# Optimization experiments

Measured on AMD Instinct MI355X. Metric: run time of the kernel, lower is better.

Reference implementation:

```python
import jax, jax.numpy as jnp
import numpy as np

ITER_ROUTING = 3
FINAL_LAMBDA = 0.01
EPS = 1e-9

N = 4
CHILD_SPACE = 12
KERNEL = 3
STRIDE = 1
CHILD_CAPS = 16
PARENT_CAPS = 32
POSE = 16


def _routing_map(child_space, k, s):
    # (child_space^2, parent_space^2) binary map: child c feeds parent p.
    parent_space = (child_space - k) // s + 1
    m = np.zeros((child_space * child_space, parent_space * parent_space), np.float32)
    for pr in range(parent_space):
        for pc in range(parent_space):
            p = pr * parent_space + pc
            for r in range(k):
                for c in range(k):
                    m[(pr * s + r) * child_space + (pc * s + c), p] = 1.0
    return m


def setup_inputs() -> dict:
    key = jax.random.key(0)
    k1, k2, k3, k4 = jax.random.split(key, 4)
    parent_space = (CHILD_SPACE - KERNEL) // STRIDE + 1
    kk = KERNEL * KERNEL
    votes = jax.random.normal(k1, (N * parent_space * parent_space, kk * CHILD_CAPS, PARENT_CAPS, POSE), jnp.float32)
    acts = jax.random.uniform(k2, (N * parent_space * parent_space, kk * CHILD_CAPS, 1), dtype=jnp.float32)
    beta_v = jax.random.normal(k3, (1, 1, 1, 1, PARENT_CAPS, 1), jnp.float32)
    beta_a = jax.random.normal(k4, (1, 1, 1, 1, PARENT_CAPS, 1), jnp.float32)
    srm = jnp.asarray(_routing_map(CHILD_SPACE, KERNEL, STRIDE))
    return {"votes_ij": votes, "activations_i": acts, "beta_v": beta_v, "beta_a": beta_a,
            "spatial_routing_matrix": srm, "batch_size": N, "kk": kk}


def _em_routing(votes_ij, activations_i, beta_v, beta_a, srm, batch_size, kk):
    Nb = batch_size
    C2, P2 = srm.shape  # child_space^2, parent_space^2
    P = int(round(P2 ** 0.5))
    K_total, O, ch = votes_ij.shape[1], votes_ij.shape[2], votes_ij.shape[3]
    child_caps = K_total // kk

    votes = votes_ij.reshape(Nb, P, P, K_total, O, ch)
    act_i = activations_i.reshape(Nb, P, P, K_total, 1, 1)

    # children per parent, ascending child index (stable argsort on -1/0 values)
    cidx = jnp.argsort(-srm, axis=0)[:kk].T           # (P2, kk)
    seg = cidx.reshape(-1)                            # (P2*kk,) child id per (parent, slot)
    ppc = jnp.sum(srm, axis=1)                        # parents-per-child, (C2,)
    # init_rr: 1 / (parents_per_child * parent_caps + 1e-9), gathered per parent slot
    rr0 = (1.0 / (ppc[cidx] * O + 1e-9)).reshape(1, P, P, kk, 1, 1)
    rr = jnp.broadcast_to(rr0, (1, P, P, kk, child_caps, O)).reshape(1, P, P, K_total, O, 1)

    layer_norm_factor = 100.0 / (float(K_total) / float(O))

    def m_step(rr, it):
        lam = FINAL_LAMBDA * (1.0 - 0.95 ** (it + 1))
        rr_prime = rr * act_i                                            # (N,P,P,K,O,1)
        rr_prime_sum = jnp.sum(rr_prime, axis=-3, keepdims=True)         # (N,P,P,1,O,1)
        mean_j = jnp.sum(rr_prime * votes, axis=-3, keepdims=True) / (rr_prime_sum + EPS)
        var_j = jnp.sum(rr_prime * jnp.square(votes - mean_j), axis=-3, keepdims=True) / (rr_prime_sum + EPS)
        cost_j_h = (beta_v + 0.5 * jnp.log(var_j + EPS)) * rr_prime_sum * layer_norm_factor
        cost_j = jnp.sum(cost_j_h, axis=-1, keepdims=True)               # (N,P,P,1,O,1)
        cost_mean = jnp.mean(cost_j, axis=-2, keepdims=True)
        cost_stdv = jnp.sqrt(jnp.sum(jnp.square(cost_j - cost_mean), axis=-2, keepdims=True) / O)
        act_j = jax.nn.sigmoid(lam * (beta_a + (cost_mean - cost_j) / (cost_stdv + EPS)))
        return act_j, mean_j, var_j

    def e_step(act_j, mean_j, var_j):
        # log N(vote; mean_j, var_j) per parent + log activation
        o_p0 = -jnp.sum(jnp.square(votes - mean_j) / (2.0 * var_j), axis=-1, keepdims=True)
        o_p2 = -0.5 * jnp.sum(jnp.log(2.0 * np.pi * var_j), axis=-1, keepdims=True)
        zz = jnp.log(act_j + EPS) + o_p0 + o_p2                          # (N,P,P,K,O,1)
        # softmax over ALL parents of each child (spatial kk slots x parent_caps),
        # done via segment reductions keyed by child id (== sparse/softmax/dense of original)
        z = jnp.moveaxis(zz.reshape(Nb, P2 * kk, child_caps, O), 1, 0)   # (P2*kk, N, cc, O)
        m = jax.ops.segment_max(jnp.max(z, axis=-1), seg, num_segments=C2)  # (C2, N, cc)
        m = jnp.where(jnp.isinf(m), 0.0, m)
        e = jnp.exp(z - m[seg][..., None])
        denom = jax.ops.segment_sum(jnp.sum(e, axis=-1), seg, num_segments=C2)
        rr_new = e / denom[seg][..., None]
        return jnp.moveaxis(rr_new, 0, 1).reshape(Nb, P, P, K_total, O, 1)

    for it in range(ITER_ROUTING):
        act_j, mean_j, var_j = m_step(rr, it)
        if it < ITER_ROUTING - 1:
            rr = e_step(act_j, mean_j, var_j)

    poses_j = mean_j[:, :, :, 0]        # (N,P,P,O,16)
    activations_j = act_j[:, :, :, 0]   # (N,P,P,O,1)
    return poses_j, activations_j


def reference(votes_ij, activations_i, beta_v, beta_a, spatial_routing_matrix, batch_size, kk):
    return _em_routing(votes_ij, activations_i, beta_v, beta_a, spatial_routing_matrix, batch_size, kk)
```

## Files before the change

kernel.cpp:

```cpp
#include <hip/hip_runtime.h>
#include <math.h>

#define NB     4
#define P      10
#define P2     100
#define CS     12
#define CCAPS  16
#define KTOT   144
#define O      32
#define POSE   16
#define VSZ    73728
#define EPSF   1e-9f
#define LNF    22.2222222222222222f
#define TWO_PI 6.28318530717958647f
#define NBP    400
#define NKQ    3
#define KPU    48
#define SUNITS (NBP*NKQ)
#define EUNITS (NB*CS*CS*2)

#define LAM0 0.0005f
#define LAM1 0.000975f
#define LAM2 0.00142625f

__device__ float g_rr [NBP*KTOT*O];
__device__ float g_zz [NBP*KTOT*O];
__device__ float g_m1 [SUNITS*512];
__device__ float g_m2 [SUNITS*512];
__device__ float g_sv [SUNITS*O];

__device__ __forceinline__ int npar(int x) {
    int a = x + 1, b = CS - x;
    int m = a < 3 ? a : 3;
    return m < b ? m : b;
}

template<bool FIRST>
__global__ __launch_bounds__(256)
void s_kernel(const float* __restrict__ votes, const float* __restrict__ acts)
{
    __shared__ float actl[KPU];
    __shared__ __align__(16) float rrp[KPU*O];
    __shared__ float4 lm1[256];
    __shared__ float4 lm2[256];
    __shared__ float  lss[256];

    const int tid = threadIdx.x;
    const int u   = blockIdx.x;
    const int bp  = u / NKQ;
    const int kq  = u - bp * NKQ;
    const int k0  = kq * KPU;
    const int ks  = tid >> 7;
    const int q   = tid & 127;
    const int o   = q >> 2;

    if (tid < KPU) actl[tid] = acts[bp * KTOT + k0 + tid];
    __syncthreads();

    for (int f = tid; f < KPU * O / 4; f += 256) {
        int kl = f >> 3;
        float4 r4;
        if (FIRST) {
            int kg = k0 + kl, kslot = kg >> 4;
            int kr = kslot / 3, kc = kslot - kr * 3;
            int p = bp % P2, pr = p / P, pc = p - pr * P;
            float ppc = (float)(npar(pr + kr) * npar(pc + kc));
            float r = actl[kl] / (ppc * 32.0f + EPSF);
            r4 = make_float4(r, r, r, r);
        } else {
            r4 = ((const float4*)(g_rr + (size_t)bp * (KTOT * O) + k0 * O))[f];
            float a = actl[kl];
            r4.x *= a; r4.y *= a; r4.z *= a; r4.w *= a;
        }
        ((float4*)rrp)[f] = r4;
    }
    __syncthreads();

    const float* vb  = votes + (size_t)bp * VSZ + (size_t)(k0 + ks * 24) * 512 + q * 4;
    const float* rr0 = rrp + (ks * 24) * O + o;
    float  s  = 0.f;
    float4 m1 = make_float4(0.f, 0.f, 0.f, 0.f);
    float4 m2 = make_float4(0.f, 0.f, 0.f, 0.f);
    #pragma unroll 8
    for (int i = 0; i < 24; ++i) {
        float  rp = rr0[i * O];
        float4 v  = *(const float4*)(vb + i * 512);
        s += rp;
        m1.x += rp * v.x;       m1.y += rp * v.y;
        m1.z += rp * v.z;       m1.w += rp * v.w;
        m2.x += rp * v.x * v.x; m2.y += rp * v.y * v.y;
        m2.z += rp * v.z * v.z; m2.w += rp * v.w * v.w;
    }
    lm1[tid] = m1; lm2[tid] = m2; lss[tid] = s;
    __syncthreads();

    if (tid < 128) {
        float4 a = lm1[tid], b = lm1[tid + 128];
        m1 = make_float4(a.x + b.x, a.y + b.y, a.z + b.z, a.w + b.w);
        a = lm2[tid]; b = lm2[tid + 128];
        m2 = make_float4(a.x + b.x, a.y + b.y, a.z + b.z, a.w + b.w);
        s = lss[tid] + lss[tid + 128];
        ((float4*)g_m1)[u * 128 + tid] = m1;
        ((float4*)g_m2)[u * 128 + tid] = m2;
        if ((tid & 3) == 0) g_sv[u * O + (tid >> 2)] = s;
    }
}

__device__ __forceinline__ void finish_bp(int bp, int tid, float lam,
                                          const float* __restrict__ beta_v,
                                          const float* __restrict__ beta_a,
                                          float4& mean, float4& i2,
                                          float& aj, float& lv2out,
                                          float* costl )
{
    const int o = tid >> 2, c4 = tid & 3;
    float4 m1 = make_float4(0.f, 0.f, 0.f, 0.f);
    float4 m2 = make_float4(0.f, 0.f, 0.f, 0.f);
    float  s  = 0.f;
    #pragma unroll
    for (int j = 0; j < NKQ; ++j) {
        float4 a = ((const float4*)g_m1)[(bp * NKQ + j) * 128 + tid];
        float4 b = ((const float4*)g_m2)[(bp * NKQ + j) * 128 + tid];
        m1.x += a.x; m1.y += a.y; m1.z += a.z; m1.w += a.w;
        m2.x += b.x; m2.y += b.y; m2.z += b.z; m2.w += b.w;
        s += g_sv[(bp * NKQ + j) * O + o];
    }
    float denom = s + EPSF;
    mean = make_float4(m1.x / denom, m1.y / denom, m1.z / denom, m1.w / denom);
    float4 var;
    var.x = fmaxf(m2.x / denom - mean.x * mean.x, 1e-30f);
    var.y = fmaxf(m2.y / denom - mean.y * mean.y, 1e-30f);
    var.z = fmaxf(m2.z / denom - mean.z * mean.z, 1e-30f);
    var.w = fmaxf(m2.w / denom - mean.w * mean.w, 1e-30f);
    i2 = make_float4(0.5f / var.x, 0.5f / var.y, 0.5f / var.z, 0.5f / var.w);
    float lve = logf(var.x + EPSF) + logf(var.y + EPSF)
              + logf(var.z + EPSF) + logf(var.w + EPSF);
    float lv2 = logf(TWO_PI * var.x) + logf(TWO_PI * var.y)
              + logf(TWO_PI * var.z) + logf(TWO_PI * var.w);
    lve += __shfl_xor(lve, 1); lve += __shfl_xor(lve, 2);
    lv2 += __shfl_xor(lv2, 1); lv2 += __shfl_xor(lv2, 2);
    lv2out = lv2;
    if (c4 == 0) costl[o] = (16.f * beta_v[o] + 0.5f * lve) * s * LNF;
    __syncthreads();
    float cm = 0.f;
    #pragma unroll
    for (int i = 0; i < O; ++i) cm += costl[i];
    cm *= (1.f / 32.f);
    float sq = 0.f;
    #pragma unroll
    for (int i = 0; i < O; ++i) { float d = costl[i] - cm; sq += d * d; }
    float cstd = sqrtf(sq * (1.f / 32.f));
    aj = 1.f / (1.f + expf(-lam * (beta_a[o] + (cm - costl[o]) / (cstd + EPSF))));
}

__global__ __launch_bounds__(256)
void zf_kernel(const float* __restrict__ votes,
               const float* __restrict__ beta_v,
               const float* __restrict__ beta_a, float lam)
{
    __shared__ float4 ml[128];
    __shared__ float4 il[128];
    __shared__ float  zl[O];
    __shared__ float  costl[O];
    __shared__ __align__(16) float zzl[KPU*O];

    const int tid = threadIdx.x;
    const int u   = blockIdx.x;
    const int bp  = u / NKQ;
    const int kq  = u - bp * NKQ;
    const int k0  = kq * KPU;
    const int ks  = tid >> 7;
    const int q   = tid & 127;
    const int o   = q >> 2;
    const int c4  = q & 3;

    {
        float4 mean, i2; float aj, lv2;
        if (tid < 128) {
            finish_bp(bp, tid, lam, beta_v, beta_a, mean, i2, aj, lv2, costl);
            ml[tid] = mean; il[tid] = i2;
            if ((tid & 3) == 0)
                zl[tid >> 2] = logf(aj + EPSF) - 0.5f * lv2;
        } else {
            __syncthreads();
        }
    }
    __syncthreads();

    const float* vb = votes + (size_t)bp * VSZ + (size_t)(k0 + ks * 24) * 512 + q * 4;
    float4 m  = ml[q];
    float4 iv = il[q];
    float  zp = zl[o];
    #pragma unroll 8
    for (int i = 0; i < 24; ++i) {
        float4 v = *(const float4*)(vb + i * 512);
        float dx = v.x - m.x, dy = v.y - m.y, dz = v.z - m.z, dw = v.w - m.w;
        float t = dx * dx * iv.x + dy * dy * iv.y + dz * dz * iv.z + dw * dw * iv.w;
        t += __shfl_xor(t, 1); t += __shfl_xor(t, 2);
        if (c4 == 0) zzl[(ks * 24 + i) * O + o] = zp - t;
    }
    __syncthreads();
    float4* dst = (float4*)(g_zz + (size_t)bp * (KTOT * O) + k0 * O);
    for (int f = tid; f < KPU * O / 4; f += 256)
        dst[f] = ((float4*)zzl)[f];
}

__global__ __launch_bounds__(256)
void f_last_kernel(const float* __restrict__ beta_v,
                   const float* __restrict__ beta_a,
                   float* __restrict__ out, float lam)
{
    __shared__ float costl[O];
    const int tid = threadIdx.x;
    const int bp  = blockIdx.x;
    float4 mean, i2; float aj, lv2;
    if (tid < 128) {
        finish_bp(bp, tid, lam, beta_v, beta_a, mean, i2, aj, lv2, costl);
        ((float4*)out)[bp * 128 + tid] = mean;
        if ((tid & 3) == 0)
            out[(size_t)NBP * 512 + bp * O + (tid >> 2)] = aj;
    } else {
        __syncthreads();
    }
}

__global__ __launch_bounds__(256)
void e_kernel()
{
    const int tid = threadIdx.x;
    const int u   = blockIdx.x;
    const int b   = u / (CS * CS * 2);
    int r = u - b * (CS * CS * 2);
    const int child = r >> 1, half = r & 1;
    const int cr = child / CS, cl = child - cr * CS;
    const int cc = half * 8 + (tid >> 5), o = tid & 31;

    float zz[9];
    float vmax = -1e30f;
    #pragma unroll
    for (int kr = 0; kr < 3; ++kr) {
        int pr_ = cr - kr;
        #pragma unroll
        for (int kc = 0; kc < 3; ++kc) {
            int pc_ = cl - kc, si = kr * 3 + kc;
            float z = -1e30f;
            if (pr_ >= 0 && pr_ < P && pc_ >= 0 && pc_ < P) {
                int bpp = b * P2 + pr_ * P + pc_;
                z = g_zz[(size_t)bpp * (KTOT * O) + (si * CCAPS + cc) * O + o];
            }
            zz[si] = z;
            vmax = fmaxf(vmax, z);
        }
    }
    vmax = fmaxf(vmax, __shfl_xor(vmax, 1));
    vmax = fmaxf(vmax, __shfl_xor(vmax, 2));
    vmax = fmaxf(vmax, __shfl_xor(vmax, 4));
    vmax = fmaxf(vmax, __shfl_xor(vmax, 8));
    vmax = fmaxf(vmax, __shfl_xor(vmax, 16));

    float ps = 0.f;
    #pragma unroll
    for (int si = 0; si < 9; ++si) {
        float e = (zz[si] > -1e29f) ? expf(zz[si] - vmax) : 0.f;
        zz[si] = e;
        ps += e;
    }
    ps += __shfl_xor(ps, 1);
    ps += __shfl_xor(ps, 2);
    ps += __shfl_xor(ps, 4);
    ps += __shfl_xor(ps, 8);
    ps += __shfl_xor(ps, 16);
    float inv = 1.f / ps;

    #pragma unroll
    for (int kr = 0; kr < 3; ++kr) {
        int pr_ = cr - kr;
        #pragma unroll
        for (int kc = 0; kc < 3; ++kc) {
            int pc_ = cl - kc, si = kr * 3 + kc;
            if (pr_ >= 0 && pr_ < P && pc_ >= 0 && pc_ < P) {
                int bpp = b * P2 + pr_ * P + pc_;
                g_rr[(size_t)bpp * (KTOT * O) + (si * CCAPS + cc) * O + o] = zz[si] * inv;
            }
        }
    }
}

extern "C" void kernel_launch(void* const* d_in, const int* in_sizes, int n_in,
                              void* d_out, int out_size, void* d_ws, size_t ws_size,
                              hipStream_t stream)
{
    (void)in_sizes; (void)n_in; (void)out_size; (void)d_ws; (void)ws_size;

    const float* votes = (const float*)d_in[0];
    const float* acts  = (const float*)d_in[1];
    const float* bv    = (const float*)d_in[2];
    const float* ba    = (const float*)d_in[3];
    float* out = (float*)d_out;

    dim3 t(256);
    s_kernel<true ><<<dim3(SUNITS), t, 0, stream>>>(votes, acts);
    zf_kernel<<<dim3(SUNITS), t, 0, stream>>>(votes, bv, ba, LAM0);
    e_kernel<<<dim3(EUNITS), t, 0, stream>>>();

    s_kernel<false><<<dim3(SUNITS), t, 0, stream>>>(votes, acts);
    zf_kernel<<<dim3(SUNITS), t, 0, stream>>>(votes, bv, ba, LAM1);
    e_kernel<<<dim3(EUNITS), t, 0, stream>>>();

    s_kernel<false><<<dim3(SUNITS), t, 0, stream>>>(votes, acts);
    f_last_kernel<<<dim3(NBP), t, 0, stream>>>(bv, ba, out, LAM2);
}
```

Before: 276.8 us.

## Cache votes as fp16 in workspace and read half-precision copy in later passes

The first M-step pass now also writes an fp16 copy of the votes tensor into the workspace. Every later pass (the z computations and the second and third M-steps) reads 8 halves per thread instead of 4 floats, so those passes move half as many bytes. Thread mapping and the reductions are reworked to fit the new 8-element vectors. The cost is lower precision in the means, variances and log-likelihoods, plus an extra fp16 write during the first pass.

Result: faster. 257.5 us (-7.0%).

```diff
diff --git a/kernel.cpp b/kernel.cpp
--- a/kernel.cpp
+++ b/kernel.cpp
@@ -1,4 +1,5 @@
 #include <hip/hip_runtime.h>
+#include <hip/hip_fp16.h>
 #include <math.h>
 
 #define NB     4
@@ -35,9 +36,18 @@
     return m < b ? m : b;
 }
 
-template<bool FIRST>
-__global__ __launch_bounds__(256)
-void s_kernel(const float* __restrict__ votes, const float* __restrict__ acts)
+__device__ __forceinline__ void up8(uint4 u, float* f) {
+    float2 a = __half22float2(*(__half2*)&u.x);
+    float2 b = __half22float2(*(__half2*)&u.y);
+    float2 c = __half22float2(*(__half2*)&u.z);
+    float2 d = __half22float2(*(__half2*)&u.w);
+    f[0] = a.x; f[1] = a.y; f[2] = b.x; f[3] = b.y;
+    f[4] = c.x; f[5] = c.y; f[6] = d.x; f[7] = d.y;
+}
+
+__global__ __launch_bounds__(256)
+void v_kernel(const float* __restrict__ votes, const float* __restrict__ acts,
+              __half* __restrict__ hv)
 {
     __shared__ float actl[KPU];
     __shared__ __align__(16) float rrp[KPU*O];
@@ -59,24 +69,17 @@
 
     for (int f = tid; f < KPU * O / 4; f += 256) {
         int kl = f >> 3;
-        float4 r4;
-        if (FIRST) {
-            int kg = k0 + kl, kslot = kg >> 4;
-            int kr = kslot / 3, kc = kslot - kr * 3;
-            int p = bp % P2, pr = p / P, pc = p - pr * P;
-            float ppc = (float)(npar(pr + kr) * npar(pc + kc));
-            float r = actl[kl] / (ppc * 32.0f + EPSF);
-            r4 = make_float4(r, r, r, r);
-        } else {
-            r4 = ((const float4*)(g_rr + (size_t)bp * (KTOT * O) + k0 * O))[f];
-            float a = actl[kl];
-            r4.x *= a; r4.y *= a; r4.z *= a; r4.w *= a;
-        }
-        ((float4*)rrp)[f] = r4;
+        int kg = k0 + kl, kslot = kg >> 4;
+        int kr = kslot / 3, kc = kslot - kr * 3;
+        int p = bp % P2, pr = p / P, pc = p - pr * P;
+        float ppc = (float)(npar(pr + kr) * npar(pc + kc));
+        float r = actl[kl] / (ppc * 32.0f + EPSF);
+        ((float4*)rrp)[f] = make_float4(r, r, r, r);
     }
     __syncthreads();
 
     const float* vb  = votes + (size_t)bp * VSZ + (size_t)(k0 + ks * 24) * 512 + q * 4;
+    __half*      hb  = hv    + (size_t)bp * VSZ + (size_t)(k0 + ks * 24) * 512 + q * 4;
     const float* rr0 = rrp + (ks * 24) * O + o;
     float  s  = 0.f;
     float4 m1 = make_float4(0.f, 0.f, 0.f, 0.f);
@@ -90,6 +93,12 @@
         m1.z += rp * v.z;       m1.w += rp * v.w;
         m2.x += rp * v.x * v.x; m2.y += rp * v.y * v.y;
         m2.z += rp * v.z * v.z; m2.w += rp * v.w * v.w;
+        __half2 ha = __floats2half2_rn(v.x, v.y);
+        __half2 hbv = __floats2half2_rn(v.z, v.w);
+        uint2 st;
+        st.x = *(unsigned int*)&ha;
+        st.y = *(unsigned int*)&hbv;
+        *(uint2*)(hb + i * 512) = st;
     }
     lm1[tid] = m1; lm2[tid] = m2; lss[tid] = s;
     __syncthreads();
@@ -103,6 +112,80 @@
         ((float4*)g_m1)[u * 128 + tid] = m1;
         ((float4*)g_m2)[u * 128 + tid] = m2;
         if ((tid & 3) == 0) g_sv[u * O + (tid >> 2)] = s;
+    }
+}
+
+__global__ __launch_bounds__(256)
+void s16_kernel(const __half* __restrict__ hv, const float* __restrict__ acts)
+{
+    __shared__ float actl[KPU];
+    __shared__ __align__(16) float rrp[KPU*O];
+    __shared__ float4 lm1[512];
+    __shared__ float4 lm2[512];
+    __shared__ float  lss[256];
+
+    const int tid = threadIdx.x;
+    const int u   = blockIdx.x;
+    const int bp  = u / NKQ;
+    const int kq  = u - bp * NKQ;
+    const int k0  = kq * KPU;
+    const int ks  = tid >> 6;
+    const int qp  = tid & 63;
+    const int o   = qp >> 1;
+
+    if (tid < KPU) actl[tid] = acts[bp * KTOT + k0 + tid];
+    __syncthreads();
+
+    for (int f = tid; f < KPU * O / 4; f += 256) {
+        int kl = f >> 3;
+        float4 r4 = ((const float4*)(g_rr + (size_t)bp * (KTOT * O) + k0 * O))[f];
+        float a = actl[kl];
+        r4.x *= a; r4.y *= a; r4.z *= a; r4.w *= a;
+        ((float4*)rrp)[f] = r4;
+    }
+    __syncthreads();
+
+    const __half* vb = hv + (size_t)bp * VSZ + (size_t)(k0 + ks * 12) * 512 + qp * 8;
+    const float* rr0 = rrp + (ks * 12) * O + o;
+    float s = 0.f;
+    float m1[8], m2[8];
+    #pragma unroll
+    for (int j = 0; j < 8; ++j) { m1[j] = 0.f; m2[j] = 0.f; }
+    #pragma unroll 4
+    for (int i = 0; i < 12; ++i) {
+        float rp = rr0[i * O];
+        uint4 u4 = *(const uint4*)(vb + i * 512);
+        float f[8]; up8(u4, f);
+        s += rp;
+        #pragma unroll
+        for (int j = 0; j < 8; ++j) {
+            m1[j] += rp * f[j];
+            m2[j] += rp * f[j] * f[j];
+        }
+    }
+    lm1[tid*2]   = make_float4(m1[0], m1[1], m1[2], m1[3]);
+    lm1[tid*2+1] = make_float4(m1[4], m1[5], m1[6], m1[7]);
+    lm2[tid*2]   = make_float4(m2[0], m2[1], m2[2], m2[3]);
+    lm2[tid*2+1] = make_float4(m2[4], m2[5], m2[6], m2[7]);
+    lss[tid] = s;
+    __syncthreads();
+
+    if (tid < 64) {
+        #pragma unroll
+        for (int j = 0; j < 2; ++j) {
+            float4 a0 = lm1[(tid)*2+j],       a1 = lm1[(64+tid)*2+j];
+            float4 a2 = lm1[(128+tid)*2+j],   a3 = lm1[(192+tid)*2+j];
+            float4 r = make_float4(a0.x+a1.x+a2.x+a3.x, a0.y+a1.y+a2.y+a3.y,
+                                   a0.z+a1.z+a2.z+a3.z, a0.w+a1.w+a2.w+a3.w);
+            ((float4*)g_m1)[u * 128 + tid*2 + j] = r;
+            float4 b0 = lm2[(tid)*2+j],       b1 = lm2[(64+tid)*2+j];
+            float4 b2 = lm2[(128+tid)*2+j],   b3 = lm2[(192+tid)*2+j];
+            float4 r2 = make_float4(b0.x+b1.x+b2.x+b3.x, b0.y+b1.y+b2.y+b3.y,
+                                    b0.z+b1.z+b2.z+b3.z, b0.w+b1.w+b2.w+b3.w);
+            ((float4*)g_m2)[u * 128 + tid*2 + j] = r2;
+        }
+        float sr = lss[tid] + lss[64+tid] + lss[128+tid] + lss[192+tid];
+        if ((tid & 1) == 0) g_sv[u * O + (tid >> 1)] = sr;
     }
 }
 
@@ -154,9 +237,9 @@
 }
 
 __global__ __launch_bounds__(256)
-void zf_kernel(const float* __restrict__ votes,
-               const float* __restrict__ beta_v,
-               const float* __restrict__ beta_a, float lam)
+void zf16_kernel(const __half* __restrict__ hv,
+                 const float* __restrict__ beta_v,
+                 const float* __restrict__ beta_a, float lam)
 {
     __shared__ float4 ml[128];
     __shared__ float4 il[128];
@@ -169,10 +252,10 @@
     const int bp  = u / NKQ;
     const int kq  = u - bp * NKQ;
     const int k0  = kq * KPU;
-    const int ks  = tid >> 7;
-    const int q   = tid & 127;
-    const int o   = q >> 2;
-    const int c4  = q & 3;
+    const int ks  = tid >> 6;
+    const int qp  = tid & 63;
+    const int o   = qp >> 1;
+    const int h   = qp & 1;
 
     {
         float4 mean, i2; float aj, lv2;
@@ -187,17 +270,20 @@
     }
     __syncthreads();
 
-    const float* vb = votes + (size_t)bp * VSZ + (size_t)(k0 + ks * 24) * 512 + q * 4;
-    float4 m  = ml[q];
-    float4 iv = il[q];
+    const __half* vb = hv + (size_t)bp * VSZ + (size_t)(k0 + ks * 12) * 512 + qp * 8;
+    float4 mA = ml[o*4 + h*2], mB = ml[o*4 + h*2 + 1];
+    float4 iA = il[o*4 + h*2], iB = il[o*4 + h*2 + 1];
     float  zp = zl[o];
-    #pragma unroll 8
-    for (int i = 0; i < 24; ++i) {
-        float4 v = *(const float4*)(vb + i * 512);
-        float dx = v.x - m.x, dy = v.y - m.y, dz = v.z - m.z, dw = v.w - m.w;
-        float t = dx * dx * iv.x + dy * dy * iv.y + dz * dz * iv.z + dw * dw * iv.w;
-        t += __shfl_xor(t, 1); t += __shfl_xor(t, 2);
-        if (c4 == 0) zzl[(ks * 24 + i) * O + o] = zp - t;
+    #pragma unroll 4
+    for (int i = 0; i < 12; ++i) {
+        uint4 u4 = *(const uint4*)(vb + i * 512);
+        float f[8]; up8(u4, f);
+        float d0 = f[0]-mA.x, d1 = f[1]-mA.y, d2 = f[2]-mA.z, d3 = f[3]-mA.w;
+        float d4 = f[4]-mB.x, d5 = f[5]-mB.y, d6 = f[6]-mB.z, d7 = f[7]-mB.w;
+        float t = d0*d0*iA.x + d1*d1*iA.y + d2*d2*iA.z + d3*d3*iA.w
+                + d4*d4*iB.x + d5*d5*iB.y + d6*d6*iB.z + d7*d7*iB.w;
+        t += __shfl_xor(t, 1);
+        if (h == 0) zzl[(ks * 12 + i) * O + o] = zp - t;
     }
     __syncthreads();
     float4* dst = (float4*)(g_zz + (size_t)bp * (KTOT * O) + k0 * O);
@@ -290,23 +376,24 @@
                               void* d_out, int out_size, void* d_ws, size_t ws_size,
                               hipStream_t stream)
 {
-    (void)in_sizes; (void)n_in; (void)out_size; (void)d_ws; (void)ws_size;
+    (void)in_sizes; (void)n_in; (void)out_size; (void)ws_size;
 
     const float* votes = (const float*)d_in[0];
     const float* acts  = (const float*)d_in[1];
     const float* bv    = (const float*)d_in[2];
     const float* ba    = (const float*)d_in[3];
     float* out = (float*)d_out;
+    __half* hv = (__half*)d_ws;
 
     dim3 t(256);
-    s_kernel<true ><<<dim3(SUNITS), t, 0, stream>>>(votes, acts);
-    zf_kernel<<<dim3(SUNITS), t, 0, stream>>>(votes, bv, ba, LAM0);
+    v_kernel<<<dim3(SUNITS), t, 0, stream>>>(votes, acts, hv);
+    zf16_kernel<<<dim3(SUNITS), t, 0, stream>>>(hv, bv, ba, LAM0);
     e_kernel<<<dim3(EUNITS), t, 0, stream>>>();
 
-    s_kernel<false><<<dim3(SUNITS), t, 0, stream>>>(votes, acts);
-    zf_kernel<<<dim3(SUNITS), t, 0, stream>>>(votes, bv, ba, LAM1);
+    s16_kernel<<<dim3(SUNITS), t, 0, stream>>>(hv, acts);
+    zf16_kernel<<<dim3(SUNITS), t, 0, stream>>>(hv, bv, ba, LAM1);
     e_kernel<<<dim3(EUNITS), t, 0, stream>>>();
 
-    s_kernel<false><<<dim3(SUNITS), t, 0, stream>>>(votes, acts);
+    s16_kernel<<<dim3(SUNITS), t, 0, stream>>>(hv, acts);
     f_last_kernel<<<dim3(NBP), t, 0, stream>>>(bv, ba, out, LAM2);
 }
```

## Fuse E-step with next M-step stats per child and cache votes as fp16

Applied to the files above, without the earlier changes.

The routing pipeline is restructured. The first pass writes an fp16 copy of votes into the workspace. A per-child kernel then computes the log-likelihood, the softmax over all parents and the weighted partial moments in one pass, so the zz and rr round trips and the separate full-precision vote re-reads go away. Small per-parent finish kernels reduce the partials. Votes are read at half the bytes in later iterations, at the cost of fp16 precision loss in mean and variance, plus extra block-wide syncs inside a loop with possibly divergent bounds.

Measured after the change: 304.7 us. 10.1% more time.

```diff
diff --git a/kernel.cpp b/kernel.cpp
--- a/kernel.cpp
+++ b/kernel.cpp
@@ -1,4 +1,5 @@
 #include <hip/hip_runtime.h>
+#include <hip/hip_fp16.h>
 #include <math.h>
 
 #define NB     4
@@ -17,17 +18,21 @@
 #define NKQ    3
 #define KPU    48
 #define SUNITS (NBP*NKQ)
-#define EUNITS (NB*CS*CS*2)
+#define NCQ    2
+#define CZG    (NB*CS*CS*NCQ)
 
 #define LAM0 0.0005f
 #define LAM1 0.000975f
 #define LAM2 0.00142625f
 
-__device__ float g_rr [NBP*KTOT*O];
-__device__ float g_zz [NBP*KTOT*O];
 __device__ float g_m1 [SUNITS*512];
 __device__ float g_m2 [SUNITS*512];
 __device__ float g_sv [SUNITS*O];
+__device__ float g_pm [NBP*9*NCQ*1024];
+__device__ float g_ps [NBP*9*NCQ*32];
+__device__ float g_mean[NBP*512];
+__device__ float g_i2v [NBP*512];
+__device__ float g_zpre[NBP*O];
 
 __device__ __forceinline__ int npar(int x) {
     int a = x + 1, b = CS - x;
@@ -35,9 +40,18 @@
     return m < b ? m : b;
 }
 
-template<bool FIRST>
+__device__ __forceinline__ void up8(uint4 u, float* f) {
+    float2 a = __half22float2(*(__half2*)&u.x);
+    float2 b = __half22float2(*(__half2*)&u.y);
+    float2 c = __half22float2(*(__half2*)&u.z);
+    float2 d = __half22float2(*(__half2*)&u.w);
+    f[0] = a.x; f[1] = a.y; f[2] = b.x; f[3] = b.y;
+    f[4] = c.x; f[5] = c.y; f[6] = d.x; f[7] = d.y;
+}
+
 __global__ __launch_bounds__(256)
-void s_kernel(const float* __restrict__ votes, const float* __restrict__ acts)
+void v_kernel(const float* __restrict__ votes, const float* __restrict__ acts,
+              __half* __restrict__ hv)
 {
     __shared__ float actl[KPU];
     __shared__ __align__(16) float rrp[KPU*O];
@@ -59,24 +73,17 @@
 
     for (int f = tid; f < KPU * O / 4; f += 256) {
         int kl = f >> 3;
-        float4 r4;
-        if (FIRST) {
-            int kg = k0 + kl, kslot = kg >> 4;
-            int kr = kslot / 3, kc = kslot - kr * 3;
-            int p = bp % P2, pr = p / P, pc = p - pr * P;
-            float ppc = (float)(npar(pr + kr) * npar(pc + kc));
-            float r = actl[kl] / (ppc * 32.0f + EPSF);
-            r4 = make_float4(r, r, r, r);
-        } else {
-            r4 = ((const float4*)(g_rr + (size_t)bp * (KTOT * O) + k0 * O))[f];
-            float a = actl[kl];
-            r4.x *= a; r4.y *= a; r4.z *= a; r4.w *= a;
-        }
-        ((float4*)rrp)[f] = r4;
+        int kg = k0 + kl, kslot = kg >> 4;
+        int kr = kslot / 3, kc = kslot - kr * 3;
+        int p = bp % P2, pr = p / P, pc = p - pr * P;
+        float ppc = (float)(npar(pr + kr) * npar(pc + kc));
+        float r = actl[kl] / (ppc * 32.0f + EPSF);
+        ((float4*)rrp)[f] = make_float4(r, r, r, r);
     }
     __syncthreads();
 
     const float* vb  = votes + (size_t)bp * VSZ + (size_t)(k0 + ks * 24) * 512 + q * 4;
+    __half*      hb  = hv    + (size_t)bp * VSZ + (size_t)(k0 + ks * 24) * 512 + q * 4;
     const float* rr0 = rrp + (ks * 24) * O + o;
     float  s  = 0.f;
     float4 m1 = make_float4(0.f, 0.f, 0.f, 0.f);
@@ -90,6 +97,12 @@
         m1.z += rp * v.z;       m1.w += rp * v.w;
         m2.x += rp * v.x * v.x; m2.y += rp * v.y * v.y;
         m2.z += rp * v.z * v.z; m2.w += rp * v.w * v.w;
+        __half2 ha  = __floats2half2_rn(v.x, v.y);
+        __half2 hbv = __floats2half2_rn(v.z, v.w);
+        uint2 st;
+        st.x = *(unsigned int*)&ha;
+        st.y = *(unsigned int*)&hbv;
+        *(uint2*)(hb + i * 512) = st;
     }
     lm1[tid] = m1; lm2[tid] = m2; lss[tid] = s;
     __syncthreads();
@@ -106,14 +119,15 @@
     }
 }
 
-__device__ __forceinline__ void finish_bp(int bp, int tid, float lam,
-                                          const float* __restrict__ beta_v,
-                                          const float* __restrict__ beta_a,
-                                          float4& mean, float4& i2,
-                                          float& aj, float& lv2out,
-                                          float* costl )
-{
+__global__ __launch_bounds__(128)
+void f0_kernel(const float* __restrict__ beta_v,
+               const float* __restrict__ beta_a, float lam)
+{
+    __shared__ float costl[O];
+    const int tid = threadIdx.x;
     const int o = tid >> 2, c4 = tid & 3;
+    const int bp = blockIdx.x;
+
     float4 m1 = make_float4(0.f, 0.f, 0.f, 0.f);
     float4 m2 = make_float4(0.f, 0.f, 0.f, 0.f);
     float  s  = 0.f;
@@ -126,129 +140,83 @@
         s += g_sv[(bp * NKQ + j) * O + o];
     }
     float denom = s + EPSF;
-    mean = make_float4(m1.x / denom, m1.y / denom, m1.z / denom, m1.w / denom);
+    float4 mean = make_float4(m1.x/denom, m1.y/denom, m1.z/denom, m1.w/denom);
     float4 var;
-    var.x = fmaxf(m2.x / denom - mean.x * mean.x, 1e-30f);
-    var.y = fmaxf(m2.y / denom - mean.y * mean.y, 1e-30f);
-    var.z = fmaxf(m2.z / denom - mean.z * mean.z, 1e-30f);
-    var.w = fmaxf(m2.w / denom - mean.w * mean.w, 1e-30f);
-    i2 = make_float4(0.5f / var.x, 0.5f / var.y, 0.5f / var.z, 0.5f / var.w);
-    float lve = logf(var.x + EPSF) + logf(var.y + EPSF)
-              + logf(var.z + EPSF) + logf(var.w + EPSF);
-    float lv2 = logf(TWO_PI * var.x) + logf(TWO_PI * var.y)
-              + logf(TWO_PI * var.z) + logf(TWO_PI * var.w);
-    lve += __shfl_xor(lve, 1); lve += __shfl_xor(lve, 2);
-    lv2 += __shfl_xor(lv2, 1); lv2 += __shfl_xor(lv2, 2);
-    lv2out = lv2;
-    if (c4 == 0) costl[o] = (16.f * beta_v[o] + 0.5f * lve) * s * LNF;
+    var.x = fmaxf(m2.x/denom - mean.x*mean.x, 1e-30f);
+    var.y = fmaxf(m2.y/denom - mean.y*mean.y, 1e-30f);
+    var.z = fmaxf(m2.z/denom - mean.z*mean.z, 1e-30f);
+    var.w = fmaxf(m2.w/denom - mean.w*mean.w, 1e-30f);
+    float4 i2 = make_float4(0.5f/var.x, 0.5f/var.y, 0.5f/var.z, 0.5f/var.w);
+    float lve = logf(var.x+EPSF)+logf(var.y+EPSF)+logf(var.z+EPSF)+logf(var.w+EPSF);
+    float lv2 = logf(TWO_PI*var.x)+logf(TWO_PI*var.y)+logf(TWO_PI*var.z)+logf(TWO_PI*var.w);
+    lve += __shfl_xor(lve,1); lve += __shfl_xor(lve,2);
+    lv2 += __shfl_xor(lv2,1); lv2 += __shfl_xor(lv2,2);
+    if (c4 == 0) costl[o] = (16.f*beta_v[o] + 0.5f*lve) * s * LNF;
     __syncthreads();
     float cm = 0.f;
     #pragma unroll
     for (int i = 0; i < O; ++i) cm += costl[i];
-    cm *= (1.f / 32.f);
+    cm *= (1.f/32.f);
     float sq = 0.f;
     #pragma unroll
-    for (int i = 0; i < O; ++i) { float d = costl[i] - cm; sq += d * d; }
-    float cstd = sqrtf(sq * (1.f / 32.f));
-    aj = 1.f / (1.f + expf(-lam * (beta_a[o] + (cm - costl[o]) / (cstd + EPSF))));
+    for (int i = 0; i < O; ++i) { float d = costl[i]-cm; sq += d*d; }
+    float cstd = sqrtf(sq * (1.f/32.f));
+    float aj = 1.f/(1.f+expf(-lam*(beta_a[o] + (cm-costl[o])/(cstd+EPSF))));
+    ((float4*)g_mean)[bp*128+tid] = mean;
+    ((float4*)g_i2v)[bp*128+tid]  = i2;
+    if (c4 == 0) g_zpre[bp*O+o] = logf(aj+EPSF) - 0.5f*lv2;
 }
 
 __global__ __launch_bounds__(256)
-void zf_kernel(const float* __restrict__ votes,
-               const float* __restrict__ beta_v,
-               const float* __restrict__ beta_a, float lam)
-{
-    __shared__ float4 ml[128];
-    __shared__ float4 il[128];
-    __shared__ float  zl[O];
-    __shared__ float  costl[O];
-    __shared__ __align__(16) float zzl[KPU*O];
+void cz_kernel(const __half* __restrict__ hv, const float* __restrict__ acts)
+{
+    __shared__ float red[4*32*33];
 
     const int tid = threadIdx.x;
-    const int u   = blockIdx.x;
-    const int bp  = u / NKQ;
-    const int kq  = u - bp * NKQ;
-    const int k0  = kq * KPU;
-    const int ks  = tid >> 7;
-    const int q   = tid & 127;
-    const int o   = q >> 2;
-    const int c4  = q & 3;
-
-    {
-        float4 mean, i2; float aj, lv2;
-        if (tid < 128) {
-            finish_bp(bp, tid, lam, beta_v, beta_a, mean, i2, aj, lv2, costl);
-            ml[tid] = mean; il[tid] = i2;
-            if ((tid & 3) == 0)
-                zl[tid >> 2] = logf(aj + EPSF) - 0.5f * lv2;
-        } else {
-            __syncthreads();
-        }
-    }
-    __syncthreads();
-
-    const float* vb = votes + (size_t)bp * VSZ + (size_t)(k0 + ks * 24) * 512 + q * 4;
-    float4 m  = ml[q];
-    float4 iv = il[q];
-    float  zp = zl[o];
-    #pragma unroll 8
-    for (int i = 0; i < 24; ++i) {
-        float4 v = *(const float4*)(vb + i * 512);
-        float dx = v.x - m.x, dy = v.y - m.y, dz = v.z - m.z, dw = v.w - m.w;
-        float t = dx * dx * iv.x + dy * dy * iv.y + dz * dz * iv.z + dw * dw * iv.w;
-        t += __shfl_xor(t, 1); t += __shfl_xor(t, 2);
-        if (c4 == 0) zzl[(ks * 24 + i) * O + o] = zp - t;
-    }
-    __syncthreads();
-    float4* dst = (float4*)(g_zz + (size_t)bp * (KTOT * O) + k0 * O);
-    for (int f = tid; f < KPU * O / 4; f += 256)
-        dst[f] = ((float4*)zzl)[f];
-}
-
-__global__ __launch_bounds__(256)
-void f_last_kernel(const float* __restrict__ beta_v,
-                   const float* __restrict__ beta_a,
-                   float* __restrict__ out, float lam)
-{
-    __shared__ float costl[O];
-    const int tid = threadIdx.x;
-    const int bp  = blockIdx.x;
-    float4 mean, i2; float aj, lv2;
-    if (tid < 128) {
-        finish_bp(bp, tid, lam, beta_v, beta_a, mean, i2, aj, lv2, costl);
-        ((float4*)out)[bp * 128 + tid] = mean;
-        if ((tid & 3) == 0)
-            out[(size_t)NBP * 512 + bp * O + (tid >> 2)] = aj;
-    } else {
-        __syncthreads();
-    }
-}
-
-__global__ __launch_bounds__(256)
-void e_kernel()
-{
-    const int tid = threadIdx.x;
-    const int u   = blockIdx.x;
-    const int b   = u / (CS * CS * 2);
-    int r = u - b * (CS * CS * 2);
-    const int child = r >> 1, half = r & 1;
-    const int cr = child / CS, cl = child - cr * CS;
-    const int cc = half * 8 + (tid >> 5), o = tid & 31;
-
-    float zz[9];
+    const int ccl = tid >> 5;
+    const int o   = tid & 31;
+    const int blk = blockIdx.x;
+    const int ccq = blk & (NCQ-1);
+    const int bc  = blk / NCQ;
+    const int b   = bc / (CS*CS);
+    const int c   = bc - b*(CS*CS);
+    const int cr  = c / CS, cl = c - cr*CS;
+    const int cc  = ccq*8 + ccl;
+
+    int   bpps[9];
+    float ez[9];
+    float av[9];
     float vmax = -1e30f;
+
     #pragma unroll
     for (int kr = 0; kr < 3; ++kr) {
-        int pr_ = cr - kr;
         #pragma unroll
         for (int kc = 0; kc < 3; ++kc) {
-            int pc_ = cl - kc, si = kr * 3 + kc;
+            const int si  = kr*3 + kc;
+            const int pr_ = cr - kr, pc_ = cl - kc;
+            const bool ok = (pr_ >= 0 && pr_ < P && pc_ >= 0 && pc_ < P);
+            int bpp = ok ? (b*P2 + pr_*P + pc_) : -1;
+            bpps[si] = bpp;
             float z = -1e30f;
-            if (pr_ >= 0 && pr_ < P && pc_ >= 0 && pc_ < P) {
-                int bpp = b * P2 + pr_ * P + pc_;
-                z = g_zz[(size_t)bpp * (KTOT * O) + (si * CCAPS + cc) * O + o];
+            if (ok) {
+                const __half* vb = hv + (size_t)bpp*VSZ + (size_t)(si*16+cc)*512 + o*16;
+                uint4 u0 = *(const uint4*)(vb);
+                uint4 u1 = *(const uint4*)(vb + 8);
+                float f[16]; up8(u0, f); up8(u1, f + 8);
+                const float4* mm = (const float4*)(g_mean + (size_t)bpp*512 + o*16);
+                const float4* iv = (const float4*)(g_i2v  + (size_t)bpp*512 + o*16);
+                float t = 0.f;
+                #pragma unroll
+                for (int j4 = 0; j4 < 4; ++j4) {
+                    float4 m = mm[j4], w = iv[j4];
+                    float d0 = f[j4*4  ]-m.x, d1 = f[j4*4+1]-m.y;
+                    float d2 = f[j4*4+2]-m.z, d3 = f[j4*4+3]-m.w;
+                    t += d0*d0*w.x + d1*d1*w.y + d2*d2*w.z + d3*d3*w.w;
+                }
+                z = g_zpre[bpp*O + o] - t;
+                av[si] = acts[bpp*KTOT + si*16 + cc];
             }
-            zz[si] = z;
+            ez[si] = z;
             vmax = fmaxf(vmax, z);
         }
     }
@@ -257,12 +225,11 @@
     vmax = fmaxf(vmax, __shfl_xor(vmax, 4));
     vmax = fmaxf(vmax, __shfl_xor(vmax, 8));
     vmax = fmaxf(vmax, __shfl_xor(vmax, 16));
-
     float ps = 0.f;
     #pragma unroll
     for (int si = 0; si < 9; ++si) {
-        float e = (zz[si] > -1e29f) ? expf(zz[si] - vmax) : 0.f;
-        zz[si] = e;
+        float e = (ez[si] > -1e29f) ? expf(ez[si] - vmax) : 0.f;
+        ez[si] = e;
         ps += e;
     }
     ps += __shfl_xor(ps, 1);
@@ -270,19 +237,114 @@
     ps += __shfl_xor(ps, 4);
     ps += __shfl_xor(ps, 8);
     ps += __shfl_xor(ps, 16);
-    float inv = 1.f / ps;
-
-    #pragma unroll
-    for (int kr = 0; kr < 3; ++kr) {
-        int pr_ = cr - kr;
+    const float inv = 1.f / ps;
+
+    #pragma unroll
+    for (int si = 0; si < 9; ++si) {
+        const int bpp = bpps[si];
+        if (bpp >= 0) {
+            float rp = ez[si] * inv * av[si];
+            const __half* vb = hv + (size_t)bpp*VSZ + (size_t)(si*16+cc)*512 + o*16;
+            uint4 u0 = *(const uint4*)(vb);
+            uint4 u1 = *(const uint4*)(vb + 8);
+            float f[16]; up8(u0, f); up8(u1, f + 8);
+            float m1[16], m2[16];
+            #pragma unroll
+            for (int j = 0; j < 16; ++j) { m1[j] = rp*f[j]; m2[j] = rp*f[j]*f[j]; }
+            float s = rp;
+            #pragma unroll
+            for (int j = 0; j < 16; ++j) {
+                m1[j] += __shfl_xor(m1[j], 32);
+                m2[j] += __shfl_xor(m2[j], 32);
+            }
+            s += __shfl_xor(s, 32);
+            if ((ccl & 1) == 0) {
+                float* r = red + ((ccl >> 1)*32 + o)*33;
+                #pragma unroll
+                for (int j = 0; j < 16; ++j) { r[j] = m1[j]; r[16+j] = m2[j]; }
+                r[32] = s;
+            }
+            __syncthreads();
+            if (tid < 32) {
+                float* dst = g_pm + ((size_t)(bpp*9 + si)*NCQ + ccq)*1024;
+                float sa = 0.f;
+                #pragma unroll
+                for (int j4 = 0; j4 < 8; ++j4) {
+                    float4 acc = make_float4(0.f, 0.f, 0.f, 0.f);
+                    #pragma unroll
+                    for (int w = 0; w < 4; ++w) {
+                        const float* r = red + (w*32 + tid)*33 + j4*4;
+                        acc.x += r[0]; acc.y += r[1]; acc.z += r[2]; acc.w += r[3];
+                    }
+                    int half = j4 >> 2, j4l = j4 & 3;
+                    ((float4*)(dst + half*512))[tid*4 + j4l] = acc;
+                }
+                #pragma unroll
+                for (int w = 0; w < 4; ++w) sa += red[(w*32 + tid)*33 + 32];
+                g_ps[((bpp*9 + si)*NCQ + ccq)*32 + tid] = sa;
+            }
+            __syncthreads();
+        }
+    }
+}
+
+template<bool LAST>
+__global__ __launch_bounds__(128)
+void f12_kernel(const float* __restrict__ beta_v,
+                const float* __restrict__ beta_a,
+                float* __restrict__ out, float lam)
+{
+    __shared__ float costl[O];
+    const int tid = threadIdx.x;
+    const int o = tid >> 2, c4 = tid & 3;
+    const int bp = blockIdx.x;
+
+    float4 m1 = make_float4(0.f, 0.f, 0.f, 0.f);
+    float4 m2 = make_float4(0.f, 0.f, 0.f, 0.f);
+    float  s  = 0.f;
+    #pragma unroll
+    for (int si = 0; si < 9; ++si) {
         #pragma unroll
-        for (int kc = 0; kc < 3; ++kc) {
-            int pc_ = cl - kc, si = kr * 3 + kc;
-            if (pr_ >= 0 && pr_ < P && pc_ >= 0 && pc_ < P) {
-                int bpp = b * P2 + pr_ * P + pc_;
-                g_rr[(size_t)bpp * (KTOT * O) + (si * CCAPS + cc) * O + o] = zz[si] * inv;
-            }
+        for (int qq = 0; qq < NCQ; ++qq) {
+            const float* base = g_pm + ((size_t)(bp*9 + si)*NCQ + qq)*1024;
+            float4 a = ((const float4*)base)[tid];
+            float4 b = ((const float4*)(base + 512))[tid];
+            m1.x += a.x; m1.y += a.y; m1.z += a.z; m1.w += a.w;
+            m2.x += b.x; m2.y += b.y; m2.z += b.z; m2.w += b.w;
+            s += g_ps[((bp*9 + si)*NCQ + qq)*32 + o];
         }
+    }
+    float denom = s + EPSF;
+    float4 mean = make_float4(m1.x/denom, m1.y/denom, m1.z/denom, m1.w/denom);
+    float4 var;
+    var.x = fmaxf(m2.x/denom - mean.x*mean.x, 1e-30f);
+    var.y = fmaxf(m2.y/denom - mean.y*mean.y, 1e-30f);
+    var.z = fmaxf(m2.z/denom - mean.z*mean.z, 1e-30f);
+    var.w = fmaxf(m2.w/denom - mean.w*mean.w, 1e-30f);
+    float4 i2 = make_float4(0.5f/var.x, 0.5f/var.y, 0.5f/var.z, 0.5f/var.w);
+    float lve = logf(var.x+EPSF)+logf(var.y+EPSF)+logf(var.z+EPSF)+logf(var.w+EPSF);
+    float lv2 = logf(TWO_PI*var.x)+logf(TWO_PI*var.y)+logf(TWO_PI*var.z)+logf(TWO_PI*var.w);
+    lve += __shfl_xor(lve,1); lve += __shfl_xor(lve,2);
+    lv2 += __shfl_xor(lv2,1); lv2 += __shfl_xor(lv2,2);
+    if (c4 == 0) costl[o] = (16.f*beta_v[o] + 0.5f*lve) * s * LNF;
+    __syncthreads();
+    float cm = 0.f;
+    #pragma unroll
+    for (int i = 0; i < O; ++i) cm += costl[i];
+    cm *= (1.f/32.f);
+    float sq = 0.f;
+    #pragma unroll
+    for (int i = 0; i < O; ++i) { float d = costl[i]-cm; sq += d*d; }
+    float cstd = sqrtf(sq * (1.f/32.f));
+    float aj = 1.f/(1.f+expf(-lam*(beta_a[o] + (cm-costl[o])/(cstd+EPSF))));
+
+    if (LAST) {
+        ((float4*)out)[bp*128 + tid] = mean;
+        if (c4 == 0) out[(size_t)NBP*512 + bp*O + o] = aj;
+    } else {
+        ((float4*)g_mean)[bp*128 + tid] = mean;
+        ((float4*)g_i2v)[bp*128 + tid]  = i2;
+        if (c4 == 0) g_zpre[bp*O + o] = logf(aj+EPSF) - 0.5f*lv2;
     }
 }
 
@@ -290,23 +352,19 @@
                               void* d_out, int out_size, void* d_ws, size_t ws_size,
                               hipStream_t stream)
 {
-    (void)in_sizes; (void)n_in; (void)out_size; (void)d_ws; (void)ws_size;
+    (void)in_sizes; (void)n_in; (void)out_size; (void)ws_size;
 
     const float* votes = (const float*)d_in[0];
     const float* acts  = (const float*)d_in[1];
     const float* bv    = (const float*)d_in[2];
     const float* ba    = (const float*)d_in[3];
     float* out = (float*)d_out;
-
-    dim3 t(256);
-    s_kernel<true ><<<dim3(SUNITS), t, 0, stream>>>(votes, acts);
-    zf_kernel<<<dim3(SUNITS), t, 0, stream>>>(votes, bv, ba, LAM0);
-    e_kernel<<<dim3(EUNITS), t, 0, stream>>>();
-
-    s_kernel<false><<<dim3(SUNITS), t, 0, stream>>>(votes, acts);
-    zf_kernel<<<dim3(SUNITS), t, 0, stream>>>(votes, bv, ba, LAM1);
-    e_kernel<<<dim3(EUNITS), t, 0, stream>>>();
-
-    s_kernel<false><<<dim3(SUNITS), t, 0, stream>>>(votes, acts);
-    f_last_kernel<<<dim3(NBP), t, 0, stream>>>(bv, ba, out, LAM2);
-}
+    __half* hv = (__half*)d_ws;
+
+    v_kernel<<<dim3(SUNITS), dim3(256), 0, stream>>>(votes, acts, hv);
+    f0_kernel<<<dim3(NBP), dim3(128), 0, stream>>>(bv, ba, LAM0);
+    cz_kernel<<<dim3(CZG), dim3(256), 0, stream>>>(hv, acts);
+    f12_kernel<false><<<dim3(NBP), dim3(128), 0, stream>>>(bv, ba, out, LAM1);
+    cz_kernel<<<dim3(CZG), dim3(256), 0, stream>>>(hv, acts);
+    f12_kernel<true ><<<dim3(NBP), dim3(128), 0, stream>>>(bv, ba, out, LAM2);
+}
```
